# Kernel tuning notes

Hardware: AMD Instinct MI355X
Metric: run time of the kernel (lower is better)

## Reference

```python
import jax, jax.numpy as jnp
import numpy as np

RES = 64          # img_resolution
SIGMA = 1.0       # Gaussian kernel sigma
PI = RES * RES    # flattened persistence image size
B, P0, P1 = 256, 1024, 512
EPS_P = 1e-6
EPS_D = 1e-8
LN_EPS = 1e-5


def setup_inputs() -> dict:
    key = jax.random.key(0)
    ks = jax.random.split(key, 8)
    pairs_h0 = jax.random.uniform(ks[0], (B, P0, 2), dtype=jnp.float32)
    pairs_h1 = jax.random.uniform(ks[1], (B, P1, 2), dtype=jnp.float32)
    W1 = jax.random.normal(ks[2], (2 * PI, 512), dtype=jnp.float32) * 0.02
    W2 = jax.random.normal(ks[3], (512, 256), dtype=jnp.float32) * 0.02
    W3 = jax.random.normal(ks[4], (256, 128), dtype=jnp.float32) * 0.02
    return dict(
        pairs_h0=pairs_h0, pairs_h1=pairs_h1,
        W1=W1, b1=jnp.zeros((512,), jnp.float32), g1=jnp.ones((512,), jnp.float32), be1=jnp.zeros((512,), jnp.float32),
        W2=W2, b2=jnp.zeros((256,), jnp.float32), g2=jnp.ones((256,), jnp.float32), be2=jnp.zeros((256,), jnp.float32),
        W3=W3, b3=jnp.zeros((128,), jnp.float32),
    )


def _masked_minmax(x, valid):
    big = jnp.float32(1e30)
    mn = jnp.min(jnp.where(valid, x, big))
    mx = jnp.max(jnp.where(valid, x, -big))
    degen = (mx - mn) < 1e-6
    mn = jnp.where(degen, 0.0, mn)
    mx = jnp.where(degen, 1.0, mx)
    return mn, mx


def _pers_image(pairs):
    """pairs: [P, 2] (birth, death) -> [RES, RES] persistence image."""
    births = pairs[:, 0]
    pers = pairs[:, 1] - pairs[:, 0]
    valid = pers > EPS_P
    any_valid = jnp.any(valid)
    bmin, bmax = _masked_minmax(births, valid)
    pmin, pmax = _masked_minmax(pers, valid)
    bn = (births - bmin) / (bmax - bmin + EPS_D)   # [P]
    pn = (pers - pmin) / (pmax - pmin + EPS_D)     # [P]
    w = jnp.where(valid, pers, 0.0)                # weight = persistence, invalid -> 0
    grid = jnp.linspace(0.0, 1.0, RES)
    inv2s2 = 1.0 / (2.0 * SIGMA * SIGMA)
    kb = jnp.exp(-((grid[None, :] - bn[:, None]) ** 2) * inv2s2)  # [P, RES] over b_grid
    kp = jnp.exp(-((grid[None, :] - pn[:, None]) ** 2) * inv2s2)  # [P, RES] over p_grid
    # img[i, j] = sum_p w_p * exp(-(bdiff_p[i] + pdiff_p[j]) / 2s^2)  (separable Gaussian)
    img = jnp.einsum('p,pi,pj->ij', w, kb, kp)
    return jnp.where(any_valid, img, jnp.zeros_like(img))


def _layernorm(x, g, b):
    mu = jnp.mean(x, axis=-1, keepdims=True)
    var = jnp.mean((x - mu) ** 2, axis=-1, keepdims=True)
    return (x - mu) * jax.lax.rsqrt(var + LN_EPS) * g + b


def reference(pairs_h0, pairs_h1, W1, b1, g1, be1, W2, b2, g2, be2, W3, b3):
    bsz = pairs_h0.shape[0]
    pi0 = jax.vmap(_pers_image)(pairs_h0).reshape(bsz, -1)  # [B, RES*RES]
    pi1 = jax.vmap(_pers_image)(pairs_h1).reshape(bsz, -1)
    feats = jnp.concatenate([pi0, pi1], axis=1)             # [B, 2*PI]
    h = jax.nn.relu(_layernorm(feats @ W1 + b1, g1, be1))   # dropout: eval mode (identity)
    h = jax.nn.relu(_layernorm(h @ W2 + b2, g2, be2))
    return h @ W3 + b3
```

## Files before the change

### kernel.cpp

```cpp
#include <hip/hip_runtime.h>
#include <hip/hip_bf16.h>
#include <hip/hip_fp16.h>


#define P0_N 1024
#define P1_N 512

typedef _Float16 h2 __attribute__((ext_vector_type(2)));
typedef _Float16 f16x8 __attribute__((ext_vector_type(8)));
typedef float f32x4 __attribute__((ext_vector_type(4)));

#define KSCALE 0.849321804f
#define DG (KSCALE / 63.0f)

static __device__ __forceinline__ float fast_exp2(float x) {
#if defined(__has_builtin)
#if __has_builtin(__builtin_amdgcn_exp2f)
    return __builtin_amdgcn_exp2f(x);
#else
    return exp2f(x);
#endif
#else
    return exp2f(x);
#endif
}

static __device__ __forceinline__ h2 pk2(float a, float b) {
#if defined(__has_builtin)
#if __has_builtin(__builtin_amdgcn_cvt_pkrtz)
    return __builtin_bit_cast(h2, __builtin_amdgcn_cvt_pkrtz(a, b));
#else
    h2 r; r[0] = (_Float16)a; r[1] = (_Float16)b; return r;
#endif
#else
    h2 r; r[0] = (_Float16)a; r[1] = (_Float16)b; return r;
#endif
}

__global__ __launch_bounds__(256) void pi_kernel(const float* __restrict__ p0,
                                                 const float* __restrict__ p1,
                                                 _Float16* __restrict__ featsH)
{
    const int task = blockIdx.x;
    const int b    = task >> 1;
    const int hom  = task & 1;
    const int P    = hom ? P1_N : P0_N;
    const float* pairs = hom ? (p1 + (size_t)b * P1_N * 2)
                             : (p0 + (size_t)b * P0_N * 2);
    const int t = threadIdx.x;
    const int w = t >> 6, lane = t & 63;

    __shared__ float cbs[1024], cps[1024], cws[1024];
    __shared__ __align__(16) _Float16 kbT[64][72];
    __shared__ __align__(16) _Float16 kpT[64][72];
    __shared__ float wmn0[4], wmx0[4], wmn1[4], wmx1[4];
    __shared__ unsigned gcnt[16];

    float bv_[4], pv_[4];
    bool  val[4];
    float bmin = 1e30f, bmax = -1e30f, pmin = 1e30f, pmax = -1e30f;
    #pragma unroll
    for (int s = 0; s < 4; ++s) {
        const int p = t + s * 256;
        val[s] = false; bv_[s] = 0.0f; pv_[s] = 0.0f;
        if (p < P) {
            const float2 pr = ((const float2*)pairs)[p];
            const float birth = pr.x;
            const float pers  = pr.y - pr.x;
            bv_[s] = birth; pv_[s] = pers;
            val[s] = pers > 1e-6f;
            if (val[s]) {
                bmin = fminf(bmin, birth); bmax = fmaxf(bmax, birth);
                pmin = fminf(pmin, pers);  pmax = fmaxf(pmax, pers);
            }
        }
    }
    #pragma unroll
    for (int d = 32; d > 0; d >>= 1) {
        bmin = fminf(bmin, __shfl_xor(bmin, d));
        bmax = fmaxf(bmax, __shfl_xor(bmax, d));
        pmin = fminf(pmin, __shfl_xor(pmin, d));
        pmax = fmaxf(pmax, __shfl_xor(pmax, d));
    }
    unsigned long long msk[4];
    #pragma unroll
    for (int s = 0; s < 4; ++s) msk[s] = __ballot(val[s]);
    if (lane == 0) {
        wmn0[w] = bmin; wmx0[w] = bmax; wmn1[w] = pmin; wmx1[w] = pmax;
        #pragma unroll
        for (int s = 0; s < 4; ++s) gcnt[w * 4 + s] = (unsigned)__popcll(msk[s]);
    }
    __syncthreads();
    float bmn = fminf(fminf(wmn0[0], wmn0[1]), fminf(wmn0[2], wmn0[3]));
    float bmx = fmaxf(fmaxf(wmx0[0], wmx0[1]), fmaxf(wmx0[2], wmx0[3]));
    float pmn = fminf(fminf(wmn1[0], wmn1[1]), fminf(wmn1[2], wmn1[3]));
    float pmx = fmaxf(fmaxf(wmx1[0], wmx1[1]), fmaxf(wmx1[2], wmx1[3]));
    if (bmx - bmn < 1e-6f) { bmn = 0.0f; bmx = 1.0f; }
    if (pmx - pmn < 1e-6f) { pmn = 0.0f; pmx = 1.0f; }
    const float binv = KSCALE / (bmx - bmn + 1e-8f);
    const float pinv = KSCALE / (pmx - pmn + 1e-8f);

    unsigned gb[4] = {0, 0, 0, 0};
    unsigned run = 0;
    #pragma unroll
    for (int g = 0; g < 16; ++g) {
        #pragma unroll
        for (int s = 0; s < 4; ++s)
            if (g == w * 4 + s) gb[s] = run;
        run += gcnt[g];
    }
    const int nv = (int)run;
    const int nchunks = (nv + 63) >> 6;

    const unsigned long long below = (1ull << lane) - 1ull;
    #pragma unroll
    for (int s = 0; s < 4; ++s) {
        if (val[s]) {
            const unsigned pos = gb[s] + (unsigned)__popcll(msk[s] & below);
            cbs[pos] = (bv_[s] - bmn) * binv;
            cps[pos] = (pv_[s] - pmn) * pinv;
            cws[pos] = pv_[s];
        }
    }
    for (int i = nv + t; i < nchunks * 64; i += 256) {
        cbs[i] = 0.0f; cps[i] = 0.0f; cws[i] = 0.0f;
    }

    const int surf = t >> 7;
    const int rem  = t & 127;
    const int po   = rem & 7;
    const int cq   = rem >> 3;
    const float G0   = (float)(cq * 4) * DG;
    const float rho  = fast_exp2(-2.0f * DG * DG);
    const float c1q  = -DG * DG * (float)(8 * cq + 1);
    const float* Xarr = surf ? cps : cbs;
    _Float16* sT = surf ? &kpT[0][0] : &kbT[0][0];

    const int wm = (w >> 1) * 32, wn = (w & 1) * 32;
    const int fr = lane & 15, fg = lane >> 4;

    f32x4 acc[2][2] = {};

    __syncthreads();
    for (int c = 0; c < nchunks; ++c) {
        const int base = c * 64;
        {
            float v[8], r[8];
            #pragma unroll
            for (int p = 0; p < 8; ++p) {
                const float X = Xarr[base + po * 8 + p];
                const float W = surf ? 1.0f : cws[base + po * 8 + p];
                const float d = G0 - X;
                v[p] = W * fast_exp2(-(d * d));
                r[p] = fast_exp2(c1q + 2.0f * DG * X);
            }
            #pragma unroll
            for (int cc = 0; cc < 4; ++cc) {
                union { uint4 u; h2 h[4]; } pk;
                pk.h[0] = pk2(v[0], v[1]);
                pk.h[1] = pk2(v[2], v[3]);
                pk.h[2] = pk2(v[4], v[5]);
                pk.h[3] = pk2(v[6], v[7]);
                *(uint4*)&sT[(cq * 4 + cc) * 72 + po * 8] = pk.u;
                #pragma unroll
                for (int p = 0; p < 8; ++p) { v[p] *= r[p]; r[p] *= rho; }
            }
        }
        __syncthreads();
        #pragma unroll
        for (int ks2 = 0; ks2 < 64; ks2 += 32) {
            f16x8 af[2], bf[2];
            af[0] = *(const f16x8*)&kbT[wm + fr][ks2 + fg * 8];
            af[1] = *(const f16x8*)&kbT[wm + 16 + fr][ks2 + fg * 8];
            bf[0] = *(const f16x8*)&kpT[wn + fr][ks2 + fg * 8];
            bf[1] = *(const f16x8*)&kpT[wn + 16 + fr][ks2 + fg * 8];
            #pragma unroll
            for (int i = 0; i < 2; ++i)
                #pragma unroll
                for (int j = 0; j < 2; ++j)
                    acc[i][j] = __builtin_amdgcn_mfma_f32_16x16x32_f16(
                        af[i], bf[j], acc[i][j], 0, 0, 0);
        }
        __syncthreads();
    }

    _Float16* dst = featsH + (size_t)b * 8192 + hom * 4096;
    #pragma unroll
    for (int i = 0; i < 2; ++i)
        #pragma unroll
        for (int j = 0; j < 2; ++j) {
            const int r0_ = wm + i * 16 + fg * 4;
            const int cc  = wn + j * 16 + fr;
            #pragma unroll
            for (int r = 0; r < 4; ++r)
                dst[(size_t)(r0_ + r) * 64 + cc] = (_Float16)acc[i][j][r];
        }
}

__global__ __launch_bounds__(256) void gemm1_mfma(const _Float16* __restrict__ Ah,
                                                  const float* __restrict__ W1,
                                                  float* __restrict__ part)
{
    const int mt = blockIdx.x;
    const int nt = blockIdx.y;
    const int ks = blockIdx.z;
    const int t  = threadIdx.x;

    __shared__ _Float16 As[64][72];
    __shared__ _Float16 Bs[64][72];

    const int mbase = mt * 64, nbase = nt * 64, kbase = ks * 512;
    const int lrow = t >> 2, lk0 = (t & 3) * 16;
    const int k0s  = (t >> 4) * 4, nc = (t & 15) * 4;

    const _Float16* Ap = Ah + (size_t)(mbase + lrow) * 8192 + kbase + lk0;
    const float*    Wp = W1 + (size_t)(kbase + k0s) * 512 + nbase + nc;

    const int w = t >> 6, lane = t & 63;
    const int wm = (w >> 1) * 32, wn = (w & 1) * 32;
    const int fr = lane & 15, fg = lane >> 4;

    f32x4 acc[2][2] = {};

    uint4  pa0 = *(const uint4*)(Ap);
    uint4  pa1 = *(const uint4*)(Ap + 8);
    float4 pw0 = *(const float4*)(Wp);
    float4 pw1 = *(const float4*)(Wp + 512);
    float4 pw2 = *(const float4*)(Wp + 1024);
    float4 pw3 = *(const float4*)(Wp + 1536);

    for (int k0 = 0; k0 < 512; k0 += 64) {
        __syncthreads();
        *(uint4*)&As[lrow][lk0]     = pa0;
        *(uint4*)&As[lrow][lk0 + 8] = pa1;
        {
            union { uint2 u; h2 h[2]; } pk;
            pk.h[0] = pk2(pw0.x, pw1.x); pk.h[1] = pk2(pw2.x, pw3.x);
            *(uint2*)&Bs[nc + 0][k0s] = pk.u;
            pk.h[0] = pk2(pw0.y, pw1.y); pk.h[1] = pk2(pw2.y, pw3.y);
            *(uint2*)&Bs[nc + 1][k0s] = pk.u;
            pk.h[0] = pk2(pw0.z, pw1.z); pk.h[1] = pk2(pw2.z, pw3.z);
            *(uint2*)&Bs[nc + 2][k0s] = pk.u;
            pk.h[0] = pk2(pw0.w, pw1.w); pk.h[1] = pk2(pw2.w, pw3.w);
            *(uint2*)&Bs[nc + 3][k0s] = pk.u;
        }
        __syncthreads();
        if (k0 + 64 < 512) {
            pa0 = *(const uint4*)(Ap + k0 + 64);
            pa1 = *(const uint4*)(Ap + k0 + 72);
            const float* wn_ = Wp + (size_t)(k0 + 64) * 512;
            pw0 = *(const float4*)(wn_);
            pw1 = *(const float4*)(wn_ + 512);
            pw2 = *(const float4*)(wn_ + 1024);
            pw3 = *(const float4*)(wn_ + 1536);
        }
        #pragma unroll
        for (int ks2 = 0; ks2 < 64; ks2 += 32) {
            f16x8 af[2], bf[2];
            af[0] = *(const f16x8*)&As[wm + fr][ks2 + fg * 8];
            af[1] = *(const f16x8*)&As[wm + 16 + fr][ks2 + fg * 8];
            bf[0] = *(const f16x8*)&Bs[wn + fr][ks2 + fg * 8];
            bf[1] = *(const f16x8*)&Bs[wn + 16 + fr][ks2 + fg * 8];
            #pragma unroll
            for (int i = 0; i < 2; ++i)
                #pragma unroll
                for (int j = 0; j < 2; ++j)
                    acc[i][j] = __builtin_amdgcn_mfma_f32_16x16x32_f16(
                        af[i], bf[j], acc[i][j], 0, 0, 0);
        }
    }

    #pragma unroll
    for (int i = 0; i < 2; ++i)
        #pragma unroll
        for (int j = 0; j < 2; ++j) {
            const int r0 = mbase + wm + i * 16 + fg * 4;
            const int c  = nbase + wn + j * 16 + fr;
            float* dst = part + (size_t)ks * (256 * 512) + (size_t)r0 * 512 + c;
            #pragma unroll
            for (int r = 0; r < 4; ++r) dst[(size_t)r * 512] = acc[i][j][r];
        }
}

__global__ __launch_bounds__(1024) void tail_kernel(const float* __restrict__ part,
    const float* __restrict__ b1, const float* __restrict__ g1, const float* __restrict__ be1,
    const float* __restrict__ W2, const float* __restrict__ b2, const float* __restrict__ g2, const float* __restrict__ be2,
    const float* __restrict__ W3, const float* __restrict__ b3,
    float* __restrict__ out)
{
    const int row  = blockIdx.x;
    const int t    = threadIdx.x;
    const int wid  = t >> 6, lane = t & 63;

    __shared__ float h1s[512];
    __shared__ float h2s[256];
    __shared__ float red[1024];
    __shared__ __align__(16) float red4[1024][4];
    __shared__ float wredA[16], wredB[16];

    const int col = t & 511, sb8 = (t >> 9) * 8;
    float v = 0.0f;
    #pragma unroll
    for (int s = 0; s < 8; ++s)
        v += part[(size_t)(sb8 + s) * (256 * 512) + (size_t)row * 512 + col];
    red[t] = v;
    __syncthreads();
    float x = 0.0f;
    if (t < 512) x = red[t] + red[t + 512] + b1[col];

    float s1 = (t < 512) ? x : 0.0f;
    float s2 = (t < 512) ? x * x : 0.0f;
    #pragma unroll
    for (int d = 32; d > 0; d >>= 1) {
        s1 += __shfl_xor(s1, d);
        s2 += __shfl_xor(s2, d);
    }
    if (lane == 0) { wredA[wid] = s1; wredB[wid] = s2; }
    __syncthreads();
    float mu = 0.0f, m2 = 0.0f;
    #pragma unroll
    for (int i = 0; i < 16; ++i) { mu += wredA[i]; m2 += wredB[i]; }
    mu *= (1.0f / 512.0f);
    m2  = m2 * (1.0f / 512.0f) - mu * mu;
    const float rs = rsqrtf(m2 + 1e-5f);
    if (t < 512) h1s[col] = fmaxf((x - mu) * rs * g1[col] + be1[col], 0.0f);
    __syncthreads();

    const int cg2 = t & 63, ksl = t >> 6;
    {
        float4 a4 = make_float4(0.0f, 0.0f, 0.0f, 0.0f);
        const float* w2p = W2 + (size_t)(ksl * 32) * 256 + cg2 * 4;
        const float* h1p = h1s + ksl * 32;
        #pragma unroll 8
        for (int k = 0; k < 32; ++k) {
            const float4 wv = *(const float4*)(w2p + (size_t)k * 256);
            const float hv = h1p[k];
            a4.x += hv * wv.x; a4.y += hv * wv.y;
            a4.z += hv * wv.z; a4.w += hv * wv.w;
        }
        *(float4*)red4[t] = a4;
    }
    __syncthreads();
    float y = 0.0f;
    if (t < 256) {
        const float* r4f = (const float*)red4;
        const int base = (t >> 2) * 4 + (t & 3);
        #pragma unroll
        for (int s = 0; s < 16; ++s) y += r4f[s * 256 + base];
        y += b2[t];
    }

    s1 = (t < 256) ? y : 0.0f;
    s2 = (t < 256) ? y * y : 0.0f;
    #pragma unroll
    for (int d = 32; d > 0; d >>= 1) {
        s1 += __shfl_xor(s1, d);
        s2 += __shfl_xor(s2, d);
    }
    if (lane == 0) { wredA[wid] = s1; wredB[wid] = s2; }
    __syncthreads();
    mu = 0.0f; m2 = 0.0f;
    #pragma unroll
    for (int i = 0; i < 16; ++i) { mu += wredA[i]; m2 += wredB[i]; }
    mu *= (1.0f / 256.0f);
    m2  = m2 * (1.0f / 256.0f) - mu * mu;
    const float rs2 = rsqrtf(m2 + 1e-5f);
    if (t < 256) h2s[t] = fmaxf((y - mu) * rs2 * g2[t] + be2[t], 0.0f);
    __syncthreads();

    const int col3 = t & 127, ks3 = t >> 7;
    float o = 0.0f;
    #pragma unroll 8
    for (int k = 0; k < 32; ++k)
        o += h2s[ks3 * 32 + k] * W3[(size_t)(ks3 * 32 + k) * 128 + col3];
    red[t] = o;
    __syncthreads();
    if (t < 128) {
        float oo = 0.0f;
        #pragma unroll
        for (int s = 0; s < 8; ++s) oo += red[t + s * 128];
        out[(size_t)row * 128 + t] = oo + b3[t];
    }
}

extern "C" void kernel_launch(void* const* d_in, const int* in_sizes, int n_in,
                              void* d_out, int out_size, void* d_ws, size_t ws_size,
                              hipStream_t stream)
{
    const float* p0  = (const float*)d_in[0];
    const float* p1  = (const float*)d_in[1];
    const float* W1  = (const float*)d_in[2];
    const float* b1  = (const float*)d_in[3];
    const float* g1  = (const float*)d_in[4];
    const float* be1 = (const float*)d_in[5];
    const float* W2  = (const float*)d_in[6];
    const float* b2  = (const float*)d_in[7];
    const float* g2  = (const float*)d_in[8];
    const float* be2 = (const float*)d_in[9];
    const float* W3  = (const float*)d_in[10];
    const float* b3  = (const float*)d_in[11];
    float* out = (float*)d_out;

    _Float16* featsH = (_Float16*)d_ws;
    float*    part   = (float*)((char*)d_ws + (4u << 20));

    hipLaunchKernelGGL(pi_kernel,    dim3(512),      dim3(256),  0, stream, p0, p1, featsH);
    hipLaunchKernelGGL(gemm1_mfma,   dim3(4, 8, 16), dim3(256),  0, stream, featsH, W1, part);
    hipLaunchKernelGGL(tail_kernel,  dim3(256),      dim3(1024), 0, stream, part,
                       b1, g1, be1, W2, b2, g2, be2, W3, b3, out);
}
```

Baseline: 42.20 us.

## Double-buffer kernel tiles in PI kernel and batch four rows per tail block

The persistence-image kernel now double-buffers its shared-memory kernel tiles. It generates the next chunk while MFMA consumes the current one, which removes one barrier per chunk. The tail kernel now handles four rows per block, so each W2/W3 weight load is reused across four rows and the grid drops from 256 to 64 blocks. The tail also sums 16 split-K partials, where it previously summed 8 twice. The trade-offs are more LDS use and fewer blocks in the tail, which may lower parallelism.

```diff
diff --git a/kernel.cpp b/kernel.cpp
--- a/kernel.cpp
+++ b/kernel.cpp
@@ -51,8 +51,8 @@
     const int w = t >> 6, lane = t & 63;
 
     __shared__ float cbs[1024], cps[1024], cws[1024];
-    __shared__ __align__(16) _Float16 kbT[64][72];
-    __shared__ __align__(16) _Float16 kpT[64][72];
+    __shared__ __align__(16) _Float16 kbT[2][64][72];
+    __shared__ __align__(16) _Float16 kpT[2][64][72];
     __shared__ float wmn0[4], wmx0[4], wmn1[4], wmx1[4];
     __shared__ unsigned gcnt[16];
 
@@ -134,46 +134,44 @@
     const float rho  = fast_exp2(-2.0f * DG * DG);
     const float c1q  = -DG * DG * (float)(8 * cq + 1);
     const float* Xarr = surf ? cps : cbs;
-    _Float16* sT = surf ? &kpT[0][0] : &kbT[0][0];
 
     const int wm = (w >> 1) * 32, wn = (w & 1) * 32;
     const int fr = lane & 15, fg = lane >> 4;
 
     f32x4 acc[2][2] = {};
 
-    __syncthreads();
-    for (int c = 0; c < nchunks; ++c) {
+    auto gen_chunk = [&](int c, int bi) {
         const int base = c * 64;
-        {
-            float v[8], r[8];
+        _Float16* sT = surf ? &kpT[bi][0][0] : &kbT[bi][0][0];
+        float v[8], r[8];
+        #pragma unroll
+        for (int p = 0; p < 8; ++p) {
+            const float X = Xarr[base + po * 8 + p];
+            const float W = surf ? 1.0f : cws[base + po * 8 + p];
+            const float d = G0 - X;
+            v[p] = W * fast_exp2(-(d * d));
+            r[p] = fast_exp2(c1q + 2.0f * DG * X);
+        }
+        #pragma unroll
+        for (int cc = 0; cc < 4; ++cc) {
+            union { uint4 u; h2 h[4]; } pk;
+            pk.h[0] = pk2(v[0], v[1]);
+            pk.h[1] = pk2(v[2], v[3]);
+            pk.h[2] = pk2(v[4], v[5]);
+            pk.h[3] = pk2(v[6], v[7]);
+            *(uint4*)&sT[(cq * 4 + cc) * 72 + po * 8] = pk.u;
             #pragma unroll
-            for (int p = 0; p < 8; ++p) {
-                const float X = Xarr[base + po * 8 + p];
-                const float W = surf ? 1.0f : cws[base + po * 8 + p];
-                const float d = G0 - X;
-                v[p] = W * fast_exp2(-(d * d));
-                r[p] = fast_exp2(c1q + 2.0f * DG * X);
-            }
-            #pragma unroll
-            for (int cc = 0; cc < 4; ++cc) {
-                union { uint4 u; h2 h[4]; } pk;
-                pk.h[0] = pk2(v[0], v[1]);
-                pk.h[1] = pk2(v[2], v[3]);
-                pk.h[2] = pk2(v[4], v[5]);
-                pk.h[3] = pk2(v[6], v[7]);
-                *(uint4*)&sT[(cq * 4 + cc) * 72 + po * 8] = pk.u;
-                #pragma unroll
-                for (int p = 0; p < 8; ++p) { v[p] *= r[p]; r[p] *= rho; }
-            }
-        }
-        __syncthreads();
+            for (int p = 0; p < 8; ++p) { v[p] *= r[p]; r[p] *= rho; }
+        }
+    };
+    auto consume_chunk = [&](int bi) {
         #pragma unroll
         for (int ks2 = 0; ks2 < 64; ks2 += 32) {
             f16x8 af[2], bf[2];
-            af[0] = *(const f16x8*)&kbT[wm + fr][ks2 + fg * 8];
-            af[1] = *(const f16x8*)&kbT[wm + 16 + fr][ks2 + fg * 8];
-            bf[0] = *(const f16x8*)&kpT[wn + fr][ks2 + fg * 8];
-            bf[1] = *(const f16x8*)&kpT[wn + 16 + fr][ks2 + fg * 8];
+            af[0] = *(const f16x8*)&kbT[bi][wm + fr][ks2 + fg * 8];
+            af[1] = *(const f16x8*)&kbT[bi][wm + 16 + fr][ks2 + fg * 8];
+            bf[0] = *(const f16x8*)&kpT[bi][wn + fr][ks2 + fg * 8];
+            bf[1] = *(const f16x8*)&kpT[bi][wn + 16 + fr][ks2 + fg * 8];
             #pragma unroll
             for (int i = 0; i < 2; ++i)
                 #pragma unroll
@@ -181,6 +179,14 @@
                     acc[i][j] = __builtin_amdgcn_mfma_f32_16x16x32_f16(
                         af[i], bf[j], acc[i][j], 0, 0, 0);
         }
+    };
+
+    __syncthreads();
+    if (nchunks > 0) gen_chunk(0, 0);
+    __syncthreads();
+    for (int c = 0; c < nchunks; ++c) {
+        if (c + 1 < nchunks) gen_chunk(c + 1, (c + 1) & 1);
+        consume_chunk(c & 1);
         __syncthreads();
     }
 
@@ -288,28 +294,28 @@
     const float* __restrict__ W3, const float* __restrict__ b3,
     float* __restrict__ out)
 {
-    const int row  = blockIdx.x;
+    const int rb   = blockIdx.x;
     const int t    = threadIdx.x;
     const int wid  = t >> 6, lane = t & 63;
 
-    __shared__ float h1s[512];
-    __shared__ float h2s[256];
-    __shared__ float red[1024];
-    __shared__ __align__(16) float red4[1024][4];
+    __shared__ __align__(16) float h1s4[512][4];
+    __shared__ __align__(16) float h2s4[256][4];
+    __shared__ float red[16][16][64];
     __shared__ float wredA[16], wredB[16];
 
-    const int col = t & 511, sb8 = (t >> 9) * 8;
-    float v = 0.0f;
-    #pragma unroll
-    for (int s = 0; s < 8; ++s)
-        v += part[(size_t)(sb8 + s) * (256 * 512) + (size_t)row * 512 + col];
-    red[t] = v;
-    __syncthreads();
-    float x = 0.0f;
-    if (t < 512) x = red[t] + red[t + 512] + b1[col];
-
-    float s1 = (t < 512) ? x : 0.0f;
-    float s2 = (t < 512) ? x * x : 0.0f;
+    const int r = t >> 8, col = t & 255;
+    const int row = rb * 4 + r;
+    float x0 = 0.0f, x1 = 0.0f;
+    #pragma unroll
+    for (int s = 0; s < 16; ++s) {
+        const float* pp = part + (size_t)s * (256 * 512) + (size_t)row * 512;
+        x0 += pp[col];
+        x1 += pp[col + 256];
+    }
+    x0 += b1[col];
+    x1 += b1[col + 256];
+
+    float s1 = x0 + x1, s2 = x0 * x0 + x1 * x1;
     #pragma unroll
     for (int d = 32; d > 0; d >>= 1) {
         s1 += __shfl_xor(s1, d);
@@ -319,67 +325,96 @@
     __syncthreads();
     float mu = 0.0f, m2 = 0.0f;
     #pragma unroll
-    for (int i = 0; i < 16; ++i) { mu += wredA[i]; m2 += wredB[i]; }
+    for (int i = 0; i < 4; ++i) { mu += wredA[r * 4 + i]; m2 += wredB[r * 4 + i]; }
     mu *= (1.0f / 512.0f);
     m2  = m2 * (1.0f / 512.0f) - mu * mu;
     const float rs = rsqrtf(m2 + 1e-5f);
-    if (t < 512) h1s[col] = fmaxf((x - mu) * rs * g1[col] + be1[col], 0.0f);
-    __syncthreads();
-
-    const int cg2 = t & 63, ksl = t >> 6;
+    h1s4[col][r]       = fmaxf((x0 - mu) * rs * g1[col]       + be1[col],       0.0f);
+    h1s4[col + 256][r] = fmaxf((x1 - mu) * rs * g1[col + 256] + be1[col + 256], 0.0f);
+    __syncthreads();
+
     {
-        float4 a4 = make_float4(0.0f, 0.0f, 0.0f, 0.0f);
-        const float* w2p = W2 + (size_t)(ksl * 32) * 256 + cg2 * 4;
-        const float* h1p = h1s + ksl * 32;
+        const int cg = lane, ksl = wid;
+        float4 a4[4] = {};
+        const float* w2p = W2 + (size_t)(ksl * 32) * 256 + cg * 4;
         #pragma unroll 8
         for (int k = 0; k < 32; ++k) {
             const float4 wv = *(const float4*)(w2p + (size_t)k * 256);
-            const float hv = h1p[k];
-            a4.x += hv * wv.x; a4.y += hv * wv.y;
-            a4.z += hv * wv.z; a4.w += hv * wv.w;
-        }
-        *(float4*)red4[t] = a4;
-    }
-    __syncthreads();
+            const float4 hv = *(const float4*)&h1s4[ksl * 32 + k][0];
+            a4[0].x += hv.x * wv.x; a4[0].y += hv.x * wv.y; a4[0].z += hv.x * wv.z; a4[0].w += hv.x * wv.w;
+            a4[1].x += hv.y * wv.x; a4[1].y += hv.y * wv.y; a4[1].z += hv.y * wv.z; a4[1].w += hv.y * wv.w;
+            a4[2].x += hv.z * wv.x; a4[2].y += hv.z * wv.y; a4[2].z += hv.z * wv.z; a4[2].w += hv.z * wv.w;
+            a4[3].x += hv.w * wv.x; a4[3].y += hv.w * wv.y; a4[3].z += hv.w * wv.z; a4[3].w += hv.w * wv.w;
+        }
+        #pragma unroll
+        for (int rr = 0; rr < 4; ++rr) {
+            red[ksl][rr * 4 + 0][cg] = a4[rr].x;
+            red[ksl][rr * 4 + 1][cg] = a4[rr].y;
+            red[ksl][rr * 4 + 2][cg] = a4[rr].z;
+            red[ksl][rr * 4 + 3][cg] = a4[rr].w;
+        }
+    }
+    __syncthreads();
+
     float y = 0.0f;
-    if (t < 256) {
-        const float* r4f = (const float*)red4;
-        const int base = (t >> 2) * 4 + (t & 3);
-        #pragma unroll
-        for (int s = 0; s < 16; ++s) y += r4f[s * 256 + base];
-        y += b2[t];
-    }
-
-    s1 = (t < 256) ? y : 0.0f;
-    s2 = (t < 256) ? y * y : 0.0f;
+    {
+        const int cg2 = col >> 2, c2 = col & 3;
+        #pragma unroll
+        for (int s = 0; s < 16; ++s) y += red[s][r * 4 + c2][cg2];
+        y += b2[col];
+    }
+    s1 = y; s2 = y * y;
     #pragma unroll
     for (int d = 32; d > 0; d >>= 1) {
         s1 += __shfl_xor(s1, d);
         s2 += __shfl_xor(s2, d);
     }
+    __syncthreads();
     if (lane == 0) { wredA[wid] = s1; wredB[wid] = s2; }
     __syncthreads();
     mu = 0.0f; m2 = 0.0f;
     #pragma unroll
-    for (int i = 0; i < 16; ++i) { mu += wredA[i]; m2 += wredB[i]; }
+    for (int i = 0; i < 4; ++i) { mu += wredA[r * 4 + i]; m2 += wredB[r * 4 + i]; }
     mu *= (1.0f / 256.0f);
     m2  = m2 * (1.0f / 256.0f) - mu * mu;
     const float rs2 = rsqrtf(m2 + 1e-5f);
-    if (t < 256) h2s[t] = fmaxf((y - mu) * rs2 * g2[t] + be2[t], 0.0f);
-    __syncthreads();
-
-    const int col3 = t & 127, ks3 = t >> 7;
-    float o = 0.0f;
-    #pragma unroll 8
-    for (int k = 0; k < 32; ++k)
-        o += h2s[ks3 * 32 + k] * W3[(size_t)(ks3 * 32 + k) * 128 + col3];
-    red[t] = o;
-    __syncthreads();
-    if (t < 128) {
-        float oo = 0.0f;
-        #pragma unroll
-        for (int s = 0; s < 8; ++s) oo += red[t + s * 128];
-        out[(size_t)row * 128 + t] = oo + b3[t];
+    h2s4[col][r] = fmaxf((y - mu) * rs2 * g2[col] + be2[col], 0.0f);
+    __syncthreads();
+
+    {
+        const int cg3 = lane & 31;
+        const int ksx = wid * 2 + (lane >> 5);
+        float4 o4[4] = {};
+        const float* w3p = W3 + (size_t)(ksx * 8) * 128 + cg3 * 4;
+        #pragma unroll
+        for (int k = 0; k < 8; ++k) {
+            const float4 wv = *(const float4*)(w3p + (size_t)k * 128);
+            const float4 hv = *(const float4*)&h2s4[ksx * 8 + k][0];
+            o4[0].x += hv.x * wv.x; o4[0].y += hv.x * wv.y; o4[0].z += hv.x * wv.z; o4[0].w += hv.x * wv.w;
+            o4[1].x += hv.y * wv.x; o4[1].y += hv.y * wv.y; o4[1].z += hv.y * wv.z; o4[1].w += hv.y * wv.w;
+            o4[2].x += hv.z * wv.x; o4[2].y += hv.z * wv.y; o4[2].z += hv.z * wv.z; o4[2].w += hv.z * wv.w;
+            o4[3].x += hv.w * wv.x; o4[3].y += hv.w * wv.y; o4[3].z += hv.w * wv.z; o4[3].w += hv.w * wv.w;
+        }
+        float* redf = &red[0][0][0];
+        #pragma unroll
+        for (int rr = 0; rr < 4; ++rr) {
+            redf[(ksx * 16 + rr * 4 + 0) * 32 + cg3] = o4[rr].x;
+            redf[(ksx * 16 + rr * 4 + 1) * 32 + cg3] = o4[rr].y;
+            redf[(ksx * 16 + rr * 4 + 2) * 32 + cg3] = o4[rr].z;
+            redf[(ksx * 16 + rr * 4 + 3) * 32 + cg3] = o4[rr].w;
+        }
+    }
+    __syncthreads();
+
+    if (t < 512) {
+        const int r3 = t >> 7, col3 = t & 127;
+        const int cg3 = col3 >> 2, c3 = col3 & 3;
+        const float* redf = &red[0][0][0];
+        float o = 0.0f;
+        #pragma unroll
+        for (int s = 0; s < 32; ++s)
+            o += redf[(s * 16 + r3 * 4 + c3) * 32 + cg3];
+        out[(size_t)(rb * 4 + r3) * 128 + col3] = o + b3[col3];
     }
 }
 
@@ -406,6 +441,6 @@
 
     hipLaunchKernelGGL(pi_kernel,    dim3(512),      dim3(256),  0, stream, p0, p1, featsH);
     hipLaunchKernelGGL(gemm1_mfma,   dim3(4, 8, 16), dim3(256),  0, stream, featsH, W1, part);
-    hipLaunchKernelGGL(tail_kernel,  dim3(256),      dim3(1024), 0, stream, part,
+    hipLaunchKernelGGL(tail_kernel,  dim3(64),       dim3(1024), 0, stream, part,
                        b1, g1, be1, W2, b2, g2, be2, W3, b3, out);
 }
```

After: 44.53 us. +5.5%, slower.

## Compute Gaussian kernel fragments directly in registers, removing LDS staging and barriers

Applied to the files above, without the earlier changes.

The persistence-image kernel no longer builds the kb/kp Gaussian tables cooperatively in shared memory with per-chunk barriers. Each lane now computes its own MFMA A/B fragment values from the normalized point coordinates and feeds them straight into the matrix instructions. This removes the LDS tile writes and reads and the two __syncthreads per chunk. In exchange it gives up the recurrence trick that produced four grid columns per exp, so each wave evaluates more exp2 calls, and the same values are recomputed redundantly across waves.

```diff
diff --git a/kernel.cpp b/kernel.cpp
--- a/kernel.cpp
+++ b/kernel.cpp
@@ -50,9 +50,8 @@
     const int t = threadIdx.x;
     const int w = t >> 6, lane = t & 63;
 
-    __shared__ float cbs[1024], cps[1024], cws[1024];
-    __shared__ __align__(16) _Float16 kbT[64][72];
-    __shared__ __align__(16) _Float16 kpT[64][72];
+    __shared__ __align__(16) float2 cbp[1024];
+    __shared__ float cw[1024];
     __shared__ float wmn0[4], wmx0[4], wmn1[4], wmx1[4];
     __shared__ unsigned gcnt[16];
 
@@ -117,71 +116,53 @@
     for (int s = 0; s < 4; ++s) {
         if (val[s]) {
             const unsigned pos = gb[s] + (unsigned)__popcll(msk[s] & below);
-            cbs[pos] = (bv_[s] - bmn) * binv;
-            cps[pos] = (pv_[s] - pmn) * pinv;
-            cws[pos] = pv_[s];
+            cbp[pos] = make_float2((bv_[s] - bmn) * binv, (pv_[s] - pmn) * pinv);
+            cw[pos]  = pv_[s];
         }
     }
     for (int i = nv + t; i < nchunks * 64; i += 256) {
-        cbs[i] = 0.0f; cps[i] = 0.0f; cws[i] = 0.0f;
-    }
-
-    const int surf = t >> 7;
-    const int rem  = t & 127;
-    const int po   = rem & 7;
-    const int cq   = rem >> 3;
-    const float G0   = (float)(cq * 4) * DG;
-    const float rho  = fast_exp2(-2.0f * DG * DG);
-    const float c1q  = -DG * DG * (float)(8 * cq + 1);
-    const float* Xarr = surf ? cps : cbs;
-    _Float16* sT = surf ? &kpT[0][0] : &kbT[0][0];
+        cbp[i] = make_float2(0.0f, 0.0f);
+        cw[i]  = 0.0f;
+    }
+    __syncthreads();
 
     const int wm = (w >> 1) * 32, wn = (w & 1) * 32;
     const int fr = lane & 15, fg = lane >> 4;
 
+    const float Gb0 = (float)(wm + fr) * DG;
+    const float Gb1 = (float)(wm + 16 + fr) * DG;
+    const float Gp0 = (float)(wn + fr) * DG;
+    const float Gp1 = (float)(wn + 16 + fr) * DG;
+
     f32x4 acc[2][2] = {};
 
-    __syncthreads();
     for (int c = 0; c < nchunks; ++c) {
-        const int base = c * 64;
-        {
-            float v[8], r[8];
+        #pragma unroll
+        for (int hf = 0; hf < 2; ++hf) {
+            const int q0 = c * 64 + hf * 32 + fg * 8;
+            union { f16x8 v; h2 h[4]; } af0, af1, bf0, bf1;
             #pragma unroll
-            for (int p = 0; p < 8; ++p) {
-                const float X = Xarr[base + po * 8 + p];
-                const float W = surf ? 1.0f : cws[base + po * 8 + p];
-                const float d = G0 - X;
-                v[p] = W * fast_exp2(-(d * d));
-                r[p] = fast_exp2(c1q + 2.0f * DG * X);
+            for (int e2 = 0; e2 < 4; ++e2) {
+                const float4 bp = *(const float4*)&cbp[q0 + e2 * 2];
+                const float2 ww = *(const float2*)&cw[q0 + e2 * 2];
+                const float db00 = Gb0 - bp.x, db01 = Gb0 - bp.z;
+                const float db10 = Gb1 - bp.x, db11 = Gb1 - bp.z;
+                const float dp00 = Gp0 - bp.y, dp01 = Gp0 - bp.w;
+                const float dp10 = Gp1 - bp.y, dp11 = Gp1 - bp.w;
+                af0.h[e2] = pk2(ww.x * fast_exp2(-(db00 * db00)),
+                                ww.y * fast_exp2(-(db01 * db01)));
+                af1.h[e2] = pk2(ww.x * fast_exp2(-(db10 * db10)),
+                                ww.y * fast_exp2(-(db11 * db11)));
+                bf0.h[e2] = pk2(fast_exp2(-(dp00 * dp00)),
+                                fast_exp2(-(dp01 * dp01)));
+                bf1.h[e2] = pk2(fast_exp2(-(dp10 * dp10)),
+                                fast_exp2(-(dp11 * dp11)));
             }
-            #pragma unroll
-            for (int cc = 0; cc < 4; ++cc) {
-                union { uint4 u; h2 h[4]; } pk;
-                pk.h[0] = pk2(v[0], v[1]);
-                pk.h[1] = pk2(v[2], v[3]);
-                pk.h[2] = pk2(v[4], v[5]);
-                pk.h[3] = pk2(v[6], v[7]);
-                *(uint4*)&sT[(cq * 4 + cc) * 72 + po * 8] = pk.u;
-                #pragma unroll
-                for (int p = 0; p < 8; ++p) { v[p] *= r[p]; r[p] *= rho; }
-            }
-        }
-        __syncthreads();
-        #pragma unroll
-        for (int ks2 = 0; ks2 < 64; ks2 += 32) {
-            f16x8 af[2], bf[2];
-            af[0] = *(const f16x8*)&kbT[wm + fr][ks2 + fg * 8];
-            af[1] = *(const f16x8*)&kbT[wm + 16 + fr][ks2 + fg * 8];
-            bf[0] = *(const f16x8*)&kpT[wn + fr][ks2 + fg * 8];
-            bf[1] = *(const f16x8*)&kpT[wn + 16 + fr][ks2 + fg * 8];
-            #pragma unroll
-            for (int i = 0; i < 2; ++i)
-                #pragma unroll
-                for (int j = 0; j < 2; ++j)
-                    acc[i][j] = __builtin_amdgcn_mfma_f32_16x16x32_f16(
-                        af[i], bf[j], acc[i][j], 0, 0, 0);
-        }
-        __syncthreads();
+            acc[0][0] = __builtin_amdgcn_mfma_f32_16x16x32_f16(af0.v, bf0.v, acc[0][0], 0, 0, 0);
+            acc[0][1] = __builtin_amdgcn_mfma_f32_16x16x32_f16(af0.v, bf1.v, acc[0][1], 0, 0, 0);
+            acc[1][0] = __builtin_amdgcn_mfma_f32_16x16x32_f16(af1.v, bf0.v, acc[1][0], 0, 0, 0);
+            acc[1][1] = __builtin_amdgcn_mfma_f32_16x16x32_f16(af1.v, bf1.v, acc[1][1], 0, 0, 0);
+        }
     }
 
     _Float16* dst = featsH + (size_t)b * 8192 + hom * 4096;
```

Result: slower. 45.66 us (+8.2%).
